# Kernel tuning notes

Measured on AMD Instinct MI355X. Metric: run time of the kernel, lower is better.

## Reference

```python
import jax, jax.numpy as jnp
import numpy as np

NUM_HEADS = 8
WIN = 7  # local_window_size
HALF = WIN // 2


def setup_inputs() -> dict:
    key = jax.random.key(0)
    k1, k2, k3 = jax.random.split(key, 3)
    B, N, C = 1, 4096, 384  # N = T*H*W with T=4, H=W=32
    x = jax.random.normal(k1, (B, N, C), dtype=jnp.float32)
    w_qkv = jax.random.normal(k2, (C, 3 * C), dtype=jnp.float32) * 0.02
    w_proj = jax.random.normal(k3, (C, C), dtype=jnp.float32) * 0.02
    b_proj = jnp.zeros((C,), dtype=jnp.float32)
    return {"x": x, "w_qkv": w_qkv, "w_proj": w_proj, "b_proj": b_proj, "H": 32, "W": 32}


def _gather_windows(t):
    H, W = t.shape[3], t.shape[4]
    tp = jnp.pad(t, ((0, 0), (0, 0), (0, 0), (HALF, HALF), (HALF, HALF), (0, 0)))
    wins = [tp[:, :, :, dy:dy + H, dx:dx + W, :] for dy in range(WIN) for dx in range(WIN)]
    return jnp.stack(wins, axis=5)


def reference(x, w_qkv, w_proj, b_proj, H, W):
    B, N, C = x.shape
    nh, hd = NUM_HEADS, C // NUM_HEADS
    T = N // (H * W)
    scale = hd ** (-0.5)

    qkv = (x @ w_qkv).reshape(B, N, 3, nh, hd)
    # (B, nh, T, H, W, hd)
    q = qkv[:, :, 0].transpose(0, 2, 1, 3).reshape(B, nh, T, H, W, hd)
    k = qkv[:, :, 1].transpose(0, 2, 1, 3).reshape(B, nh, T, H, W, hd)
    v = qkv[:, :, 2].transpose(0, 2, 1, 3).reshape(B, nh, T, H, W, hd)

    kwin = _gather_windows(k)  # (B, nh, T, H, W, 49, hd); zeros at borders (NOT masked)
    vwin = _gather_windows(v)

    scores = jnp.einsum('bnthwd,bnthwkd->bnthwk', q, kwin) * scale
    attn = jax.nn.softmax(scores, axis=-1)  # zero-padded keys give score 0 -> weight exp(0)
    out = jnp.einsum('bnthwk,bnthwkd->bnthwd', attn, vwin)

    out = out.transpose(0, 2, 3, 4, 1, 5).reshape(B, N, C)
    return out @ w_proj + b_proj
```

## Files before the change

kernel.cpp:

```cpp
#include <hip/hip_runtime.h>
#include <hip/hip_bf16.h>
#include <math.h>

#define NH 8
#define HD 48
#define C_DIM 384
#define C3 1152

typedef unsigned short ushort_t;
typedef __attribute__((ext_vector_type(8))) short short8;
typedef __attribute__((ext_vector_type(4))) float f32x4;

__global__ __launch_bounds__(256) void split_bf16_kernel(const float* __restrict__ in,
                                                         ushort_t* __restrict__ hi,
                                                         ushort_t* __restrict__ lo,
                                                         int n4)
{
    const int i = blockIdx.x * 256 + threadIdx.x;
    if (i >= n4) return;
    const float4 v = ((const float4*)in)[i];
    const float f[4] = {v.x, v.y, v.z, v.w};
    ushort_t hb[4], lb[4];
    #pragma unroll
    for (int j = 0; j < 4; ++j) {
        __hip_bfloat16 h = __float2bfloat16(f[j]);
        __hip_bfloat16 l = __float2bfloat16(f[j] - __bfloat162float(h));
        hb[j] = *(ushort_t*)&h;
        lb[j] = *(ushort_t*)&l;
    }
    *(ushort4*)(hi + i * 4) = make_ushort4(hb[0], hb[1], hb[2], hb[3]);
    *(ushort4*)(lo + i * 4) = make_ushort4(lb[0], lb[1], lb[2], lb[3]);
}

__global__ __launch_bounds__(256) void split_wT_kernel(const float* __restrict__ w,
                                                       ushort_t* __restrict__ hiT,
                                                       ushort_t* __restrict__ loT,
                                                       int K, int N)
{
    const int idx = blockIdx.x * 256 + threadIdx.x;
    if (idx >= K * N) return;
    const int k = idx / N;
    const int n = idx - k * N;
    const float v = w[idx];
    __hip_bfloat16 h = __float2bfloat16(v);
    __hip_bfloat16 l = __float2bfloat16(v - __bfloat162float(h));
    hiT[n * K + k] = *(ushort_t*)&h;
    loT[n * K + k] = *(ushort_t*)&l;
}

__global__ __launch_bounds__(256) void gemm_mfma3(const ushort_t* __restrict__ Ah,
                                                  const ushort_t* __restrict__ Al,
                                                  const ushort_t* __restrict__ BhT,
                                                  const ushort_t* __restrict__ BlT,
                                                  const float* __restrict__ bias,
                                                  float* __restrict__ C,
                                                  int N, int K)
{
    __shared__ ushort_t sAh[128 * 40];
    __shared__ ushort_t sAl[128 * 40];
    __shared__ ushort_t sBh[64 * 40];
    __shared__ ushort_t sBl[64 * 40];

    const int tid = threadIdx.x;
    const int bm = blockIdx.x * 128;
    const int bn = blockIdx.y * 64;

    const int rowA = tid >> 2;
    const int slotA = (tid & 3) * 8;
    const int rowB = tid >> 2;
    const int slotB = (tid & 3) * 8;

    const ushort_t* gAh0 = Ah + (size_t)(bm + rowA) * K + slotA;
    const ushort_t* gAh1 = Ah + (size_t)(bm + rowA + 64) * K + slotA;
    const ushort_t* gAl0 = Al + (size_t)(bm + rowA) * K + slotA;
    const ushort_t* gAl1 = Al + (size_t)(bm + rowA + 64) * K + slotA;
    const ushort_t* gBh  = BhT + (size_t)(bn + rowB) * K + slotB;
    const ushort_t* gBl  = BlT + (size_t)(bn + rowB) * K + slotB;

    const int lane = tid & 63;
    const int wid = tid >> 6;
    const int wm = wid >> 1;
    const int wn = wid & 1;
    const int fr = lane & 15;
    const int kb = lane >> 4;
    const int aoff = (wm * 64 + fr) * 40 + kb * 8;
    const int boff = (wn * 32 + fr) * 40 + kb * 8;

    f32x4 acc[4][2] = {};

    for (int k0 = 0; k0 < K; k0 += 32) {
        const short8 va0 = *(const short8*)(gAh0 + k0);
        const short8 va1 = *(const short8*)(gAh1 + k0);
        const short8 vl0 = *(const short8*)(gAl0 + k0);
        const short8 vl1 = *(const short8*)(gAl1 + k0);
        const short8 vb0 = *(const short8*)(gBh + k0);
        const short8 vb1 = *(const short8*)(gBl + k0);
        *(short8*)&sAh[rowA * 40 + slotA]        = va0;
        *(short8*)&sAh[(rowA + 64) * 40 + slotA] = va1;
        *(short8*)&sAl[rowA * 40 + slotA]        = vl0;
        *(short8*)&sAl[(rowA + 64) * 40 + slotA] = vl1;
        *(short8*)&sBh[rowB * 40 + slotB]        = vb0;
        *(short8*)&sBl[rowB * 40 + slotB]        = vb1;
        __syncthreads();

        short8 ah[4], al[4], bh[2], bl[2];
        #pragma unroll
        for (int m = 0; m < 4; ++m) {
            ah[m] = *(const short8*)&sAh[aoff + m * 16 * 40];
            al[m] = *(const short8*)&sAl[aoff + m * 16 * 40];
        }
        #pragma unroll
        for (int n = 0; n < 2; ++n) {
            bh[n] = *(const short8*)&sBh[boff + n * 16 * 40];
            bl[n] = *(const short8*)&sBl[boff + n * 16 * 40];
        }
        #pragma unroll
        for (int m = 0; m < 4; ++m) {
            #pragma unroll
            for (int n = 0; n < 2; ++n) {
                acc[m][n] = __builtin_amdgcn_mfma_f32_16x16x32_bf16(ah[m], bh[n], acc[m][n], 0, 0, 0);
                acc[m][n] = __builtin_amdgcn_mfma_f32_16x16x32_bf16(ah[m], bl[n], acc[m][n], 0, 0, 0);
                acc[m][n] = __builtin_amdgcn_mfma_f32_16x16x32_bf16(al[m], bh[n], acc[m][n], 0, 0, 0);
            }
        }
        __syncthreads();
    }

    #pragma unroll
    for (int n = 0; n < 2; ++n) {
        const int col = bn + wn * 32 + n * 16 + fr;
        const float bv = bias ? bias[col] : 0.f;
        #pragma unroll
        for (int m = 0; m < 4; ++m) {
            const int r0 = bm + wm * 64 + m * 16 + kb * 4;
            #pragma unroll
            for (int r = 0; r < 4; ++r) {
                C[(size_t)(r0 + r) * N + col] = acc[m][n][r] + bv;
            }
        }
    }
}

__global__ __launch_bounds__(256) void gemm64(const float* __restrict__ A,
                                              const float* __restrict__ B,
                                              const float* __restrict__ bias,
                                              float* __restrict__ C,
                                              int M, int N, int K)
{
    __shared__ float As[64][17];
    __shared__ float Bs[16][64];

    const int tid = threadIdx.x;
    const int tx = tid & 15;
    const int ty = tid >> 4;
    const int bm = blockIdx.x * 64;
    const int bn = blockIdx.y * 64;
    const int arow = tid >> 2;
    const int acol = (tid & 3) << 2;
    const int brow = tid >> 4;
    const int bcol = (tid & 15) << 2;

    float acc[4][4] = {};

    for (int k0 = 0; k0 < K; k0 += 16) {
        const float4 a4 = *(const float4*)(A + (size_t)(bm + arow) * K + k0 + acol);
        const float4 b4 = *(const float4*)(B + (size_t)(k0 + brow) * N + bn + bcol);
        As[arow][acol + 0] = a4.x; As[arow][acol + 1] = a4.y;
        As[arow][acol + 2] = a4.z; As[arow][acol + 3] = a4.w;
        *(float4*)&Bs[brow][bcol] = b4;
        __syncthreads();
        #pragma unroll
        for (int kk = 0; kk < 16; ++kk) {
            const float a0 = As[ty * 4 + 0][kk];
            const float a1 = As[ty * 4 + 1][kk];
            const float a2 = As[ty * 4 + 2][kk];
            const float a3 = As[ty * 4 + 3][kk];
            const float4 b = *(const float4*)&Bs[kk][tx * 4];
            acc[0][0] = fmaf(a0, b.x, acc[0][0]); acc[0][1] = fmaf(a0, b.y, acc[0][1]);
            acc[0][2] = fmaf(a0, b.z, acc[0][2]); acc[0][3] = fmaf(a0, b.w, acc[0][3]);
            acc[1][0] = fmaf(a1, b.x, acc[1][0]); acc[1][1] = fmaf(a1, b.y, acc[1][1]);
            acc[1][2] = fmaf(a1, b.z, acc[1][2]); acc[1][3] = fmaf(a1, b.w, acc[1][3]);
            acc[2][0] = fmaf(a2, b.x, acc[2][0]); acc[2][1] = fmaf(a2, b.y, acc[2][1]);
            acc[2][2] = fmaf(a2, b.z, acc[2][2]); acc[2][3] = fmaf(a2, b.w, acc[2][3]);
            acc[3][0] = fmaf(a3, b.x, acc[3][0]); acc[3][1] = fmaf(a3, b.y, acc[3][1]);
            acc[3][2] = fmaf(a3, b.z, acc[3][2]); acc[3][3] = fmaf(a3, b.w, acc[3][3]);
        }
        __syncthreads();
    }

    float4 bb = {0.f, 0.f, 0.f, 0.f};
    if (bias) bb = *(const float4*)(bias + bn + tx * 4);
    #pragma unroll
    for (int i = 0; i < 4; ++i) {
        float4 o;
        o.x = acc[i][0] + bb.x; o.y = acc[i][1] + bb.y;
        o.z = acc[i][2] + bb.z; o.w = acc[i][3] + bb.w;
        *(float4*)(C + (size_t)(bm + ty * 4 + i) * N + bn + tx * 4) = o;
    }
}

#define KP_SHORTS 18432
#define PROW 72
__global__ __launch_bounds__(512) void local_attn_mfma2(const float* __restrict__ qkv,
                                                        ushort_t* __restrict__ outHi,
                                                        ushort_t* __restrict__ outLo)
{
    __shared__ ushort_t sKP[KP_SHORTS];
    __shared__ ushort_t sV[13504];
    __shared__ ushort_t sQ[2048];
    __shared__ float    sS[32 * 57];

    const int tid = threadIdx.x;
    const int b = blockIdx.x;
    const int t = b >> 8, h = (b >> 3) & 31, head = b & 7;
    const float scale = 0.14433756729740643f;

    if (tid < 288) {
        if (tid < 256) ((unsigned int*)(sKP + 17920))[tid] = 0u;
        else           ((unsigned int*)(sV + 13440))[tid - 256] = 0u;
    }

    #pragma unroll
    for (int it = 0; it < 4; ++it) {
        const int i = tid + it * 512;
        const int q = i >> 6, d = i & 63;
        float v = 0.f;
        if (d < 48)
            v = qkv[(size_t)((t << 10) + (h << 5) + q) * C3 + head * HD + d] * scale;
        __hip_bfloat16 bv = __float2bfloat16(v);
        sQ[q * 64 + (d ^ ((q & 7) << 3))] = *(ushort_t*)&bv;
    }
    #pragma unroll
    for (int r = 0; r < 7; ++r) {
        const int hk = h + r - 3;
        const bool rowok = (unsigned)hk < 32u;
        const size_t rk = (size_t)((t << 10) + (hk << 5)) * C3 + C_DIM + head * HD;
        #pragma unroll
        for (int it = 0; it < 5; ++it) {
            const int i = tid + it * 512;
            const int slot = i >> 6, d = i & 63;
            const int c = slot - 3;
            float v = 0.f;
            if (rowok && (unsigned)c < 32u && d < 48)
                v = qkv[rk + (size_t)c * C3 + d];
            __hip_bfloat16 bv = __float2bfloat16(v);
            sKP[(r * 40 + slot) * 64 + (d ^ ((slot & 7) << 3))] = *(ushort_t*)&bv;
        }
    }
    #pragma unroll
    for (int r = 0; r < 7; ++r) {
        const int hk = h + r - 3;
        const bool rowok = (unsigned)hk < 32u;
        const size_t rv = (size_t)((t << 10) + (hk << 5)) * C3 + 2 * C_DIM + head * HD;
        for (int i = tid; i < 1920; i += 512) {
            const int dim = i / 40;
            const int slot = i - dim * 40;
            const int c = slot - 3;
            float v = 0.f;
            if (rowok && (unsigned)c < 32u)
                v = qkv[rv + (size_t)c * C3 + dim];
            __hip_bfloat16 bv = __float2bfloat16(v);
            sV[(r * 48 + dim) * 40 + slot] = *(ushort_t*)&bv;
        }
    }
    __syncthreads();

    const int wv = tid >> 6, l = tid & 63, lr = l & 15, lc = l >> 4;

    {
        short8 aq[2][2];
        #pragma unroll
        for (int fm = 0; fm < 2; ++fm) {
            const int q = fm * 16 + lr;
            aq[fm][0] = *(const short8*)&sQ[q * 64 + ((lc * 8) ^ ((q & 7) << 3))];
            aq[fm][1] = *(const short8*)&sQ[q * 64 + ((lc * 8 + 32) ^ ((q & 7) << 3))];
        }
        for (int u = wv; u < 21; u += 8) {
            const int r = u / 3, fn = u - r * 3;
            const int slot = fn * 16 + lr;
            const short8 b0 = *(const short8*)&sKP[(r * 40 + slot) * 64 + ((lc * 8) ^ ((slot & 7) << 3))];
            const short8 b1 = *(const short8*)&sKP[(r * 40 + slot) * 64 + ((lc * 8 + 32) ^ ((slot & 7) << 3))];
            f32x4 acc0 = {}, acc1 = {};
            acc0 = __builtin_amdgcn_mfma_f32_16x16x32_bf16(aq[0][0], b0, acc0, 0, 0, 0);
            acc0 = __builtin_amdgcn_mfma_f32_16x16x32_bf16(aq[0][1], b1, acc0, 0, 0, 0);
            acc1 = __builtin_amdgcn_mfma_f32_16x16x32_bf16(aq[1][0], b0, acc1, 0, 0, 0);
            acc1 = __builtin_amdgcn_mfma_f32_16x16x32_bf16(aq[1][1], b1, acc1, 0, 0, 0);
            #pragma unroll
            for (int reg = 0; reg < 4; ++reg) {
                const int q0 = lc * 4 + reg;
                const int dx0 = slot - q0;
                if (dx0 >= 0 && dx0 < 7) sS[q0 * 57 + r * 7 + dx0] = acc0[reg];
                const int q1 = 16 + lc * 4 + reg;
                const int dx1 = slot - q1;
                if (dx1 >= 0 && dx1 < 7) sS[q1 * 57 + r * 7 + dx1] = acc1[reg];
            }
        }
    }
    __syncthreads();

    #pragma unroll
    for (int it = 0; it < 16; ++it)
        ((unsigned int*)sKP)[tid + it * 512] = 0u;
    __syncthreads();

    if (tid < 32) {
        const int q = tid;
        float sv[49];
        #pragma unroll
        for (int j = 0; j < 49; ++j) sv[j] = sS[q * 57 + j];
        float mx = sv[0];
        #pragma unroll
        for (int j = 1; j < 49; ++j) mx = fmaxf(mx, sv[j]);
        float sum = 0.f;
        #pragma unroll
        for (int j = 0; j < 49; ++j) { sv[j] = __expf(sv[j] - mx); sum += sv[j]; }
        const float inv = 1.f / sum;
        #pragma unroll
        for (int j = 0; j < 49; ++j) {
            const int r = j / 7, dx = j - (j / 7) * 7;
            __hip_bfloat16 bv = __float2bfloat16(sv[j] * inv);
            sKP[(r * 32 + q) * PROW + q + dx] = *(ushort_t*)&bv;
        }
    }
    __syncthreads();

    if (wv < 6) {
        const int fm = (wv >= 3) ? 1 : 0;
        const int fn = wv - fm * 3;
        const int q = fm * 16 + lr;
        const int dim = fn * 16 + lr;
        f32x4 acc = {};
        #pragma unroll
        for (int r = 0; r < 7; ++r) {
            const short8 a0 = *(const short8*)&sKP[(r * 32 + q) * PROW + lc * 8];
            const short8 a1 = *(const short8*)&sKP[(r * 32 + q) * PROW + lc * 8 + 32];
            const short8 b0 = *(const short8*)&sV[(r * 48 + dim) * 40 + lc * 8];
            const short8 b1 = *(const short8*)&sV[(r * 48 + dim) * 40 + lc * 8 + 32];
            acc = __builtin_amdgcn_mfma_f32_16x16x32_bf16(a0, b0, acc, 0, 0, 0);
            acc = __builtin_amdgcn_mfma_f32_16x16x32_bf16(a1, b1, acc, 0, 0, 0);
        }
        #pragma unroll
        for (int reg = 0; reg < 4; ++reg) {
            const int qq = fm * 16 + lc * 4 + reg;
            const int n = (t << 10) | (h << 5) | qq;
            const float o = acc[reg];
            __hip_bfloat16 hb = __float2bfloat16(o);
            __hip_bfloat16 lb = __float2bfloat16(o - __bfloat162float(hb));
            const size_t ob = (size_t)n * C_DIM + head * HD + dim;
            outHi[ob] = *(ushort_t*)&hb;
            outLo[ob] = *(ushort_t*)&lb;
        }
    }
}

__global__ __launch_bounds__(256) void local_attn16(const float* __restrict__ qkv,
                                                    float* __restrict__ out)
{
    const int tid = threadIdx.x;
    const int dlane = tid & 15;
    const int gid = blockIdx.x * 16 + (tid >> 4);
    const int head = gid & 7;
    const int n = gid >> 3;
    const int t = n >> 10;
    const int h = (n >> 5) & 31;
    const int w = n & 31;
    const float scale = 0.14433756729740643f;

    const float* qp = qkv + (size_t)n * C3 + head * HD;
    const float q0 = qp[dlane];
    const float q1 = qp[dlane + 16];
    const float q2 = qp[dlane + 32];

    const size_t base_k = (size_t)(C_DIM + head * HD);
    const size_t base_v = (size_t)(2 * C_DIM + head * HD);

    float s[49];
    #pragma unroll
    for (int p = 0; p < 49; ++p) {
        const int dy = p / 7, dx = p % 7;
        const int hk = h + dy - 3;
        const int wk = w + dx - 3;
        float sc = 0.f;
        if ((unsigned)hk < 32u && (unsigned)wk < 32u) {
            const int nk = (t << 10) | (hk << 5) | wk;
            const float* kp = qkv + (size_t)nk * C3 + base_k;
            float acc = q0 * kp[dlane];
            acc = fmaf(q1, kp[dlane + 16], acc);
            acc = fmaf(q2, kp[dlane + 32], acc);
            acc += __shfl_xor(acc, 1, 16);
            acc += __shfl_xor(acc, 2, 16);
            acc += __shfl_xor(acc, 4, 16);
            acc += __shfl_xor(acc, 8, 16);
            sc = acc * scale;
        }
        s[p] = sc;
    }

    float m = s[0];
    #pragma unroll
    for (int p = 1; p < 49; ++p) m = fmaxf(m, s[p]);
    float sum = 0.f;
    #pragma unroll
    for (int p = 0; p < 49; ++p) { s[p] = __expf(s[p] - m); sum += s[p]; }
    const float inv = 1.f / sum;

    float o0 = 0.f, o1 = 0.f, o2 = 0.f;
    #pragma unroll
    for (int p = 0; p < 49; ++p) {
        const int dy = p / 7, dx = p % 7;
        const int hk = h + dy - 3;
        const int wk = w + dx - 3;
        if ((unsigned)hk < 32u && (unsigned)wk < 32u) {
            const float wgt = s[p] * inv;
            const int nk = (t << 10) | (hk << 5) | wk;
            const float* vp = qkv + (size_t)nk * C3 + base_v;
            o0 = fmaf(wgt, vp[dlane],      o0);
            o1 = fmaf(wgt, vp[dlane + 16], o1);
            o2 = fmaf(wgt, vp[dlane + 32], o2);
        }
    }

    float* op = out + (size_t)n * C_DIM + head * HD;
    op[dlane]      = o0;
    op[dlane + 16] = o1;
    op[dlane + 32] = o2;
}

extern "C" void kernel_launch(void* const* d_in, const int* in_sizes, int n_in,
                              void* d_out, int out_size, void* d_ws, size_t ws_size,
                              hipStream_t stream)
{
    const float* x      = (const float*)d_in[0];
    const float* w_qkv  = (const float*)d_in[1];
    const float* w_proj = (const float*)d_in[2];
    const float* b_proj = (const float*)d_in[3];

    const int M = 4096;
    dim3 blk(256);

    const size_t NEED = 33226752;

    unsigned char* ws = (unsigned char*)d_ws;
    float* qkv = (float*)ws;
    float* att = (float*)(ws + 18874368);

    if (ws_size >= NEED) {
        ushort_t* Ah  = (ushort_t*)(ws + 25165824);
        ushort_t* Al  = (ushort_t*)(ws + 28311552);
        ushort_t* BhT = (ushort_t*)(ws + 31457280);
        ushort_t* BlT = (ushort_t*)(ws + 32342016);

        split_bf16_kernel<<<dim3(1536), blk, 0, stream>>>(x, Ah, Al, M * C_DIM / 4);
        split_wT_kernel<<<dim3((C_DIM * C3 + 255) / 256), blk, 0, stream>>>(w_qkv, BhT, BlT, C_DIM, C3);
        gemm_mfma3<<<dim3(M / 128, C3 / 64), blk, 0, stream>>>(Ah, Al, BhT, BlT, nullptr, qkv, C3, C_DIM);

        local_attn_mfma2<<<dim3(1024), dim3(512), 0, stream>>>(qkv, Ah, Al);

        split_wT_kernel<<<dim3((C_DIM * C_DIM + 255) / 256), blk, 0, stream>>>(w_proj, BhT, BlT, C_DIM, C_DIM);
        gemm_mfma3<<<dim3(M / 128, C_DIM / 64), blk, 0, stream>>>(Ah, Al, BhT, BlT, b_proj, (float*)d_out, C_DIM, C_DIM);
    } else {
        gemm64<<<dim3(M / 64, C3 / 64), blk, 0, stream>>>(x, w_qkv, nullptr, qkv, M, C3, C_DIM);
        local_attn16<<<dim3(2048), blk, 0, stream>>>(qkv, att);
        gemm64<<<dim3(M / 64, C_DIM / 64), blk, 0, stream>>>(att, w_proj, b_proj, (float*)d_out, M, C_DIM, C_DIM);
    }
}
```

Baseline: 98.33 us.

## Emit bf16 scaled QKV from GEMM epilogue and overlap sKP zeroing with softmax

The QKV GEMM now writes bf16 output directly, with the attention scale pre-applied to the Q columns. The attention kernel therefore reads half the bytes and skips the per-element float-to-bf16 conversion and scaling. The separate full shared-memory zeroing pass and its barrier are replaced by idle threads zeroing only the off-band entries while 32 threads run the softmax. The workspace layout is also compacted. The cost is that Q, K and V are rounded to bf16 after the GEMM, which the attention kernel already did before.

```diff
diff --git a/kernel.cpp b/kernel.cpp
--- a/kernel.cpp
+++ b/kernel.cpp
@@ -6,6 +6,7 @@
 #define HD 48
 #define C_DIM 384
 #define C3 1152
+#define SCALE_F 0.14433756729740643f
 
 typedef unsigned short ushort_t;
 typedef __attribute__((ext_vector_type(8))) short short8;
@@ -141,6 +142,99 @@
     }
 }
 
+__global__ __launch_bounds__(256) void gemm_mfma3_qkv(const ushort_t* __restrict__ Ah,
+                                                      const ushort_t* __restrict__ Al,
+                                                      const ushort_t* __restrict__ BhT,
+                                                      const ushort_t* __restrict__ BlT,
+                                                      ushort_t* __restrict__ Cb,
+                                                      int N, int K)
+{
+    __shared__ ushort_t sAh[128 * 40];
+    __shared__ ushort_t sAl[128 * 40];
+    __shared__ ushort_t sBh[64 * 40];
+    __shared__ ushort_t sBl[64 * 40];
+
+    const int tid = threadIdx.x;
+    const int bm = blockIdx.x * 128;
+    const int bn = blockIdx.y * 64;
+
+    const int rowA = tid >> 2;
+    const int slotA = (tid & 3) * 8;
+    const int rowB = tid >> 2;
+    const int slotB = (tid & 3) * 8;
+
+    const ushort_t* gAh0 = Ah + (size_t)(bm + rowA) * K + slotA;
+    const ushort_t* gAh1 = Ah + (size_t)(bm + rowA + 64) * K + slotA;
+    const ushort_t* gAl0 = Al + (size_t)(bm + rowA) * K + slotA;
+    const ushort_t* gAl1 = Al + (size_t)(bm + rowA + 64) * K + slotA;
+    const ushort_t* gBh  = BhT + (size_t)(bn + rowB) * K + slotB;
+    const ushort_t* gBl  = BlT + (size_t)(bn + rowB) * K + slotB;
+
+    const int lane = tid & 63;
+    const int wid = tid >> 6;
+    const int wm = wid >> 1;
+    const int wn = wid & 1;
+    const int fr = lane & 15;
+    const int kb = lane >> 4;
+    const int aoff = (wm * 64 + fr) * 40 + kb * 8;
+    const int boff = (wn * 32 + fr) * 40 + kb * 8;
+
+    f32x4 acc[4][2] = {};
+
+    for (int k0 = 0; k0 < K; k0 += 32) {
+        const short8 va0 = *(const short8*)(gAh0 + k0);
+        const short8 va1 = *(const short8*)(gAh1 + k0);
+        const short8 vl0 = *(const short8*)(gAl0 + k0);
+        const short8 vl1 = *(const short8*)(gAl1 + k0);
+        const short8 vb0 = *(const short8*)(gBh + k0);
+        const short8 vb1 = *(const short8*)(gBl + k0);
+        *(short8*)&sAh[rowA * 40 + slotA]        = va0;
+        *(short8*)&sAh[(rowA + 64) * 40 + slotA] = va1;
+        *(short8*)&sAl[rowA * 40 + slotA]        = vl0;
+        *(short8*)&sAl[(rowA + 64) * 40 + slotA] = vl1;
+        *(short8*)&sBh[rowB * 40 + slotB]        = vb0;
+        *(short8*)&sBl[rowB * 40 + slotB]        = vb1;
+        __syncthreads();
+
+        short8 ah[4], al[4], bh[2], bl[2];
+        #pragma unroll
+        for (int m = 0; m < 4; ++m) {
+            ah[m] = *(const short8*)&sAh[aoff + m * 16 * 40];
+            al[m] = *(const short8*)&sAl[aoff + m * 16 * 40];
+        }
+        #pragma unroll
+        for (int n = 0; n < 2; ++n) {
+            bh[n] = *(const short8*)&sBh[boff + n * 16 * 40];
+            bl[n] = *(const short8*)&sBl[boff + n * 16 * 40];
+        }
+        #pragma unroll
+        for (int m = 0; m < 4; ++m) {
+            #pragma unroll
+            for (int n = 0; n < 2; ++n) {
+                acc[m][n] = __builtin_amdgcn_mfma_f32_16x16x32_bf16(ah[m], bh[n], acc[m][n], 0, 0, 0);
+                acc[m][n] = __builtin_amdgcn_mfma_f32_16x16x32_bf16(ah[m], bl[n], acc[m][n], 0, 0, 0);
+                acc[m][n] = __builtin_amdgcn_mfma_f32_16x16x32_bf16(al[m], bh[n], acc[m][n], 0, 0, 0);
+            }
+        }
+        __syncthreads();
+    }
+
+    #pragma unroll
+    for (int n = 0; n < 2; ++n) {
+        const int col = bn + wn * 32 + n * 16 + fr;
+        const float sc = (col < C_DIM) ? SCALE_F : 1.0f;
+        #pragma unroll
+        for (int m = 0; m < 4; ++m) {
+            const int r0 = bm + wm * 64 + m * 16 + kb * 4;
+            #pragma unroll
+            for (int r = 0; r < 4; ++r) {
+                __hip_bfloat16 hb = __float2bfloat16(acc[m][n][r] * sc);
+                Cb[(size_t)(r0 + r) * N + col] = *(ushort_t*)&hb;
+            }
+        }
+    }
+}
+
 __global__ __launch_bounds__(256) void gemm64(const float* __restrict__ A,
                                               const float* __restrict__ B,
                                               const float* __restrict__ bias,
@@ -201,7 +295,7 @@
 
 #define KP_SHORTS 18432
 #define PROW 72
-__global__ __launch_bounds__(512) void local_attn_mfma2(const float* __restrict__ qkv,
+__global__ __launch_bounds__(512) void local_attn_mfma3(const ushort_t* __restrict__ qkvb,
                                                         ushort_t* __restrict__ outHi,
                                                         ushort_t* __restrict__ outLo)
 {
@@ -213,7 +307,6 @@
     const int tid = threadIdx.x;
     const int b = blockIdx.x;
     const int t = b >> 8, h = (b >> 3) & 31, head = b & 7;
-    const float scale = 0.14433756729740643f;
 
     if (tid < 288) {
         if (tid < 256) ((unsigned int*)(sKP + 17920))[tid] = 0u;
@@ -224,11 +317,10 @@
     for (int it = 0; it < 4; ++it) {
         const int i = tid + it * 512;
         const int q = i >> 6, d = i & 63;
-        float v = 0.f;
+        ushort_t v = 0;
         if (d < 48)
-            v = qkv[(size_t)((t << 10) + (h << 5) + q) * C3 + head * HD + d] * scale;
-        __hip_bfloat16 bv = __float2bfloat16(v);
-        sQ[q * 64 + (d ^ ((q & 7) << 3))] = *(ushort_t*)&bv;
+            v = qkvb[(size_t)((t << 10) + (h << 5) + q) * C3 + head * HD + d];
+        sQ[q * 64 + (d ^ ((q & 7) << 3))] = v;
     }
     #pragma unroll
     for (int r = 0; r < 7; ++r) {
@@ -240,11 +332,10 @@
             const int i = tid + it * 512;
             const int slot = i >> 6, d = i & 63;
             const int c = slot - 3;
-            float v = 0.f;
+            ushort_t v = 0;
             if (rowok && (unsigned)c < 32u && d < 48)
-                v = qkv[rk + (size_t)c * C3 + d];
-            __hip_bfloat16 bv = __float2bfloat16(v);
-            sKP[(r * 40 + slot) * 64 + (d ^ ((slot & 7) << 3))] = *(ushort_t*)&bv;
+                v = qkvb[rk + (size_t)c * C3 + d];
+            sKP[(r * 40 + slot) * 64 + (d ^ ((slot & 7) << 3))] = v;
         }
     }
     #pragma unroll
@@ -256,11 +347,10 @@
             const int dim = i / 40;
             const int slot = i - dim * 40;
             const int c = slot - 3;
-            float v = 0.f;
+            ushort_t v = 0;
             if (rowok && (unsigned)c < 32u)
-                v = qkv[rv + (size_t)c * C3 + dim];
-            __hip_bfloat16 bv = __float2bfloat16(v);
-            sV[(r * 48 + dim) * 40 + slot] = *(ushort_t*)&bv;
+                v = qkvb[rv + (size_t)c * C3 + dim];
+            sV[(r * 48 + dim) * 40 + slot] = v;
         }
     }
     __syncthreads();
@@ -298,11 +388,6 @@
     }
     __syncthreads();
 
-    #pragma unroll
-    for (int it = 0; it < 16; ++it)
-        ((unsigned int*)sKP)[tid + it * 512] = 0u;
-    __syncthreads();
-
     if (tid < 32) {
         const int q = tid;
         float sv[49];
@@ -320,6 +405,14 @@
             const int r = j / 7, dx = j - (j / 7) * 7;
             __hip_bfloat16 bv = __float2bfloat16(sv[j] * inv);
             sKP[(r * 32 + q) * PROW + q + dx] = *(ushort_t*)&bv;
+        }
+    } else {
+        for (int i = tid - 32; i < 7 * 32 * PROW; i += 480) {
+            const int row = i / PROW;
+            const int col = i - row * PROW;
+            const int q = row & 31;
+            if ((unsigned)(col - q) >= 7u)
+                sKP[i] = 0;
         }
     }
     __syncthreads();
@@ -364,7 +457,7 @@
     const int t = n >> 10;
     const int h = (n >> 5) & 31;
     const int w = n & 31;
-    const float scale = 0.14433756729740643f;
+    const float scale = SCALE_F;
 
     const float* qp = qkv + (size_t)n * C3 + head * HD;
     const float q0 = qp[dlane];
@@ -441,24 +534,25 @@
     const size_t NEED = 33226752;
 
     unsigned char* ws = (unsigned char*)d_ws;
-    float* qkv = (float*)ws;
-    float* att = (float*)(ws + 18874368);
 
     if (ws_size >= NEED) {
-        ushort_t* Ah  = (ushort_t*)(ws + 25165824);
-        ushort_t* Al  = (ushort_t*)(ws + 28311552);
-        ushort_t* BhT = (ushort_t*)(ws + 31457280);
-        ushort_t* BlT = (ushort_t*)(ws + 32342016);
+        ushort_t* Ah   = (ushort_t*)(ws);
+        ushort_t* Al   = (ushort_t*)(ws + 3145728);
+        ushort_t* BhT  = (ushort_t*)(ws + 6291456);
+        ushort_t* BlT  = (ushort_t*)(ws + 7176192);
+        ushort_t* qkvb = (ushort_t*)(ws + 8060928);
 
         split_bf16_kernel<<<dim3(1536), blk, 0, stream>>>(x, Ah, Al, M * C_DIM / 4);
         split_wT_kernel<<<dim3((C_DIM * C3 + 255) / 256), blk, 0, stream>>>(w_qkv, BhT, BlT, C_DIM, C3);
-        gemm_mfma3<<<dim3(M / 128, C3 / 64), blk, 0, stream>>>(Ah, Al, BhT, BlT, nullptr, qkv, C3, C_DIM);
-
-        local_attn_mfma2<<<dim3(1024), dim3(512), 0, stream>>>(qkv, Ah, Al);
+        gemm_mfma3_qkv<<<dim3(M / 128, C3 / 64), blk, 0, stream>>>(Ah, Al, BhT, BlT, qkvb, C3, C_DIM);
+
+        local_attn_mfma3<<<dim3(1024), dim3(512), 0, stream>>>(qkvb, Ah, Al);
 
         split_wT_kernel<<<dim3((C_DIM * C_DIM + 255) / 256), blk, 0, stream>>>(w_proj, BhT, BlT, C_DIM, C_DIM);
         gemm_mfma3<<<dim3(M / 128, C_DIM / 64), blk, 0, stream>>>(Ah, Al, BhT, BlT, b_proj, (float*)d_out, C_DIM, C_DIM);
     } else {
+        float* qkv = (float*)ws;
+        float* att = (float*)(ws + 18874368);
         gemm64<<<dim3(M / 64, C3 / 64), blk, 0, stream>>>(x, w_qkv, nullptr, qkv, M, C3, C_DIM);
         local_attn16<<<dim3(2048), blk, 0, stream>>>(qkv, att);
         gemm64<<<dim3(M / 64, C_DIM / 64), blk, 0, stream>>>(att, w_proj, b_proj, (float*)d_out, M, C_DIM, C_DIM);
```

Result: slower. 101.0 us (+2.7%).
